# Optimization experiments

Measured on AMD Instinct MI355X. Metric: run time of the kernel, lower is better.

## Reference

```python
import jax, jax.numpy as jnp
import numpy as np

M, N, K, D_IN = 200, 6, 25, 784
GAMMA, EPS = 0.5, 0.5
TOTAL = M * N


def setup_inputs() -> dict:
    key = jax.random.key(0)
    ks = jax.random.split(key, 8)
    B = 16384
    def lin(kk, shape, fan_in):
        bound = 1.0 / np.sqrt(fan_in)
        return jax.random.uniform(kk, shape, jnp.float32, -bound, bound)
    return {
        "batch_x": jax.random.normal(ks[0], (B, D_IN), jnp.float32),
        "Wa": lin(ks[1], (M, D_IN), D_IN),
        "ba": lin(ks[2], (M,), D_IN),
        "Wb": lin(ks[3], (TOTAL, TOTAL), TOTAL),
        "bb": lin(ks[4], (TOTAL,), TOTAL),
        "Wd": lin(ks[5], (D_IN, M), M),
        "bd": lin(ks[6], (D_IN,), M),
    }


def _step(params, carry, x):
    Wa, ba, Wb, bb, Wd, bd = params
    x_b, phi, psi = carry
    # sigma: per-group drive broadcast over cells + full recurrent term, shape (m, n)
    z_a = (Wa @ x + ba)[:, None]                      # (m, 1)
    z_b = (Wb @ x_b + bb).reshape(M, N)               # (m, n)
    sigma = z_a + z_b
    # inhibited activity
    pi = (1.0 - phi) * (sigma - sigma.min() + 1.0)    # (m, n)
    lambda_i = pi.max(axis=1)                         # (m,)
    # top-1 cell per group (scatter of topk indices == one-hot argmax)
    M_pi = jax.nn.one_hot(jnp.argmax(pi, axis=1), N, dtype=sigma.dtype)
    # top-k groups
    _, idx = jax.lax.top_k(lambda_i, K)
    M_lambda = jnp.zeros((M,), sigma.dtype).at[idx].set(1.0)[:, None]
    y = jnp.tanh(M_pi * M_lambda * sigma)             # (m, n)
    x_a_pred = Wd @ y.max(axis=1) + bd                # (D_in,)
    # memory / inhibition updates
    psi_n = jnp.maximum(EPS * psi, y)
    phi_n = jnp.maximum(GAMMA * phi, y)
    alpha = psi_n.sum()
    alpha = jnp.where(alpha == 0.0, 1.0, alpha)
    x_b_n = (psi_n / alpha).reshape(-1)
    # original detaches the recurrent state each step
    carry_n = (jax.lax.stop_gradient(x_b_n),
               jax.lax.stop_gradient(phi_n),
               jax.lax.stop_gradient(psi_n))
    return carry_n, x_a_pred


def reference(batch_x, Wa, ba, Wb, bb, Wd, bd):
    params = (Wa, ba, Wb, bb, Wd, bd)
    carry0 = (jnp.zeros((TOTAL,), batch_x.dtype),
              jnp.zeros((M, N), batch_x.dtype),
              jnp.zeros((M, N), batch_x.dtype))
    (x_b, phi, psi), preds = jax.lax.scan(
        lambda c, x: _step(params, c, x), carry0, batch_x)
    return preds, x_b, phi, psi
```

## Files before the change

### kernel.cpp

```cpp
#include <hip/hip_runtime.h>
#include <math.h>

#define Tn   16384
#define Mg   200
#define Nc   6
#define TOT  1200
#define Kk   25
#define Din  784
#define SP   28

__global__ void transpose_k(const float* __restrict__ src, float* __restrict__ dst,
                            int R, int C) {
    __shared__ float tile[32][33];
    int bx = blockIdx.x * 32, by = blockIdx.y * 32;
    int x = bx + threadIdx.x;
    for (int j = 0; j < 32; j += 8) {
        int y = by + threadIdx.y + j;
        if (x < C && y < R) tile[threadIdx.y + j][threadIdx.x] = src[(size_t)y * C + x];
    }
    __syncthreads();
    int x2 = by + threadIdx.x;
    for (int j = 0; j < 32; j += 8) {
        int y2 = bx + threadIdx.y + j;
        if (x2 < R && y2 < C) dst[(size_t)y2 * R + x2] = tile[threadIdx.x][threadIdx.y + j];
    }
}

__global__ void za_k(const float* __restrict__ X, const float* __restrict__ Wa,
                     const float* __restrict__ ba, float* __restrict__ Za) {
    __shared__ float xs[16][788];
    const int tid = threadIdx.x;
    const int t0  = blockIdx.x * 16;
    for (int idx = tid; idx < 16 * Din; idx += 256) {
        int tt = idx / Din, kk = idx - tt * Din;
        xs[tt][kk] = X[(size_t)(t0 + tt) * Din + kk];
    }
    __syncthreads();
    const int tq = tid & 15, gq = tid >> 4;
    const float4* xrow = reinterpret_cast<const float4*>(&xs[tq][0]);
    for (int g = gq; g < Mg; g += 16) {
        float acc = ba[g];
        const float4* wrow = reinterpret_cast<const float4*>(Wa + (size_t)g * Din);
        for (int k4 = 0; k4 < Din / 4; ++k4) {
            float4 a = xrow[k4], b = wrow[k4];
            acc = fmaf(a.x, b.x, acc); acc = fmaf(a.y, b.y, acc);
            acc = fmaf(a.z, b.z, acc); acc = fmaf(a.w, b.w, acc);
        }
        Za[(size_t)(t0 + tq) * Mg + g] = acc;
    }
}

__launch_bounds__(384, 1)
__global__ void serial_k(const float* __restrict__ Za, const float* __restrict__ WbT,
                         const float* __restrict__ bb,
                         unsigned long long* __restrict__ YP,
                         float* __restrict__ outTail) {
    __shared__ alignas(16) float sigma_sh[50 * SP];
    __shared__ alignas(16) float minp[8];
    __shared__ alignas(16) float selD[32];
    __shared__ alignas(16) int   selO[32];
    __shared__ float alphaS;

    const int tid  = threadIdx.x;
    const int lane = tid & 63;

    if (tid < 64) {
        const bool grp = (lane < 50);
        const int sgb  = lane * SP;
        const int cell0 = 24 * lane;
        const unsigned long long lt = (1ull << lane) - 1ull;

        float ps[24];
        #pragma unroll
        for (int i = 0; i < 24; ++i) ps[i] = 0.f;
        float alpha = 0.f;

        __syncthreads();

        for (int t = 0; t < Tn; ++t) {
            float4 mp4 = *reinterpret_cast<const float4*>(minp);
            float m = fminf(fminf(fminf(mp4.x, mp4.y), fminf(mp4.z, mp4.w)), minp[4]);
            const float m1 = 1.f - m;

            float sg[24];
            if (grp) {
                #pragma unroll
                for (int q = 0; q < 6; ++q) {
                    float4 v = *reinterpret_cast<const float4*>(sigma_sh + sgb + 4 * q);
                    sg[4*q] = v.x; sg[4*q+1] = v.y; sg[4*q+2] = v.z; sg[4*q+3] = v.w;
                }
            } else {
                #pragma unroll
                for (int i = 0; i < 24; ++i) sg[i] = 0.f;
            }

            float bs[4], bp[4]; int bj[4]; unsigned long long kb[4];
            #pragma unroll
            for (int c = 0; c < 4; ++c) { bs[c]=0.f; bp[c]=0.f; bj[c]=0; kb[c]=0ull; }
            if (grp) {
                #pragma unroll
                for (int c = 0; c < 4; ++c) {
                    float best = -INFINITY, sbv = 0.f, pbv = 0.f; int jb = 0;
                    #pragma unroll
                    for (int j = 0; j < 6; ++j) {
                        int i = 6 * c + j;
                        float pv = (1.f - ps[i]) * (sg[i] + m1);
                        bool bet = pv > best;
                        best = bet ? pv : best;
                        jb  = bet ? j : jb;
                        sbv = bet ? sg[i] : sbv;
                        pbv = bet ? ps[i] : pbv;
                    }
                    unsigned ub = __float_as_uint(best);
                    ub ^= (unsigned)(((int)ub) >> 31) | 0x80000000u;
                    int g = 4 * lane + c;
                    kb[c] = ((unsigned long long)ub << 32) |
                            (unsigned long long)(0xFFFFFFFFu - (unsigned)g);
                    bs[c] = sbv; bp[c] = pbv; bj[c] = jb;
                }
            }

            unsigned long long A = 0ull, B = ~0ull;
            unsigned long long p = __shfl(kb[0], 0);
            unsigned long long theta;
            while (true) {
                int cnt = __popcll(__ballot(kb[0] >= p)) + __popcll(__ballot(kb[1] >= p))
                        + __popcll(__ballot(kb[2] >= p)) + __popcll(__ballot(kb[3] >= p));
                if (cnt == Kk) { theta = p; break; }
                if (cnt > Kk) A = p; else B = p;
                unsigned long long m0 = __ballot(kb[0] > A && kb[0] < B);
                unsigned long long m1b = __ballot(kb[1] > A && kb[1] < B);
                unsigned long long m2 = __ballot(kb[2] > A && kb[2] < B);
                unsigned long long m3 = __ballot(kb[3] > A && kb[3] < B);
                int cls; unsigned long long mm;
                if (m0)       { cls = 0; mm = m0; }
                else if (m1b) { cls = 1; mm = m1b; }
                else if (m2)  { cls = 2; mm = m2; }
                else          { cls = 3; mm = m3; }
                int sl = __ffsll(mm) - 1;
                unsigned long long kc = (cls==0)?kb[0]:(cls==1)?kb[1]:(cls==2)?kb[2]:kb[3];
                p = __shfl(kc, sl);
            }

            unsigned long long M0 = __ballot(kb[0] >= theta);
            unsigned long long M1 = __ballot(kb[1] >= theta);
            unsigned long long M2 = __ballot(kb[2] >= theta);
            unsigned long long M3 = __ballot(kb[3] >= theta);
            int base1 = __popcll(M0);
            int base2 = base1 + __popcll(M1);
            int base3 = base2 + __popcll(M2);

            float dsum = 0.f;
            int slotr[4]; unsigned long long yv64[4];
            #pragma unroll
            for (int c = 0; c < 4; ++c) {
                slotr[c] = -1; yv64[c] = 0ull;
                unsigned long long Mc = (c==0)?M0:(c==1)?M1:(c==2)?M2:M3;
                int bse = (c==0)?0:(c==1)?base1:(c==2)?base2:base3;
                bool s = grp && (kb[c] >= theta);
                float d = 0.f;
                if (s) {
                    int slot = bse + __popcll(Mc & lt);
                    float x = fminf(fmaxf(bs[c], -9.f), 9.f);
                    float e = __expf(2.f * x);
                    float y = 1.f - 2.f / (e + 1.f);
                    float yv = fmaxf(y, 0.f);
                    d = fmaxf(y - 0.5f * bp[c], 0.f);
                    int g = 4 * lane + c;
                    selD[slot] = d;
                    selO[slot] = (6 * g + bj[c]) * TOT;
                    slotr[c] = slot;
                    yv64[c] = ((unsigned long long)(unsigned)g << 32) |
                              (unsigned long long)__float_as_uint(yv);
                }
                dsum += d;
                #pragma unroll
                for (int j = 0; j < 6; ++j) {
                    int i = 6 * c + j;
                    float add = (j == bj[c]) ? d : 0.f;
                    ps[i] = fmaf(ps[i], 0.5f, add);
                }
            }
            #pragma unroll
            for (int o = 1; o < 64; o <<= 1) dsum += __shfl_xor(dsum, o);
            alpha = fmaf(alpha, 0.5f, dsum);
            if (lane == 0) alphaS = (alpha == 0.f) ? 1.f : alpha;

            __syncthreads();
            #pragma unroll
            for (int c = 0; c < 4; ++c)
                if (slotr[c] >= 0) YP[(size_t)t * Kk + slotr[c]] = yv64[c];
            __syncthreads();
        }

        if (grp) {
            float inv2 = (alpha == 0.f) ? 1.f : (1.f / alpha);
            #pragma unroll
            for (int i = 0; i < 24; ++i) {
                outTail[cell0 + i]           = ps[i] * inv2;
                outTail[TOT + cell0 + i]     = ps[i];
                outTail[2 * TOT + cell0 + i] = ps[i];
            }
        }
    } else {
        const int j = tid - 64;
        const bool act = (j < 300);
        const int w = (tid >> 6) - 1;
        const int base = act ? 4 * j : 0;
        const int saddr = act ? ((j / 6) * SP + (4 * j) % 24) : 0;
        const int g0 = base / 6, g1 = (base + 3) / 6;
        const bool f1 = ((base + 1) / 6) != g0;
        const bool f2 = ((base + 2) / 6) != g0;
        const bool f3 = ((base + 3) / 6) != g0;

        float4 cb4 = make_float4(0.f, 0.f, 0.f, 0.f);
        if (act) cb4 = *reinterpret_cast<const float4*>(bb + base);
        float za0 = act ? Za[g0] : 0.f;
        float za1 = act ? Za[g1] : 0.f;
        float4 uo = make_float4(0.f, 0.f, 0.f, 0.f);

        {
            float s0 = cb4.x + za0;
            float s1 = cb4.y + (f1 ? za1 : za0);
            float s2 = cb4.z + (f2 ? za1 : za0);
            float s3 = cb4.w + (f3 ? za1 : za0);
            if (act)
                *reinterpret_cast<float4*>(sigma_sh + saddr) = make_float4(s0,s1,s2,s3);
            float lm = act ? fminf(fminf(s0, s1), fminf(s2, s3)) : INFINITY;
            #pragma unroll
            for (int o = 1; o < 64; o <<= 1) lm = fminf(lm, __shfl_xor(lm, o));
            if (lane == 0) minp[w] = lm;
        }
        __syncthreads();

        for (int t = 0; t < Tn; ++t) {
            const int tn = (t + 1 < Tn) ? t + 1 : t;
            float nza0 = act ? Za[(size_t)tn * Mg + g0] : 0.f;
            float nza1 = act ? Za[(size_t)tn * Mg + g1] : 0.f;
            uo.x *= 0.5f; uo.y *= 0.5f; uo.z *= 0.5f; uo.w *= 0.5f;

            __syncthreads();

            float vD = 0.f; int vO = 0;
            if (lane < 25) { vD = selD[lane]; vO = selO[lane]; }
            const float av  = alphaS;
            const float inv = 1.f / av;

            float4 cc[Kk];
            #pragma unroll
            for (int k = 0; k < Kk; ++k) {
                int offk = __builtin_amdgcn_readlane(vO, k);
                cc[k] = *reinterpret_cast<const float4*>(WbT + offk + base);
            }
            __builtin_amdgcn_sched_barrier(0);
            #pragma unroll
            for (int k = 0; k < Kk; ++k) {
                float dk = __uint_as_float(
                    (unsigned)__builtin_amdgcn_readlane((int)__float_as_uint(vD), k));
                uo.x = fmaf(dk, cc[k].x, uo.x);
                uo.y = fmaf(dk, cc[k].y, uo.y);
                uo.z = fmaf(dk, cc[k].z, uo.z);
                uo.w = fmaf(dk, cc[k].w, uo.w);
            }

            float s0 = fmaf(uo.x, inv, cb4.x + nza0);
            float s1 = fmaf(uo.y, inv, cb4.y + (f1 ? nza1 : nza0));
            float s2 = fmaf(uo.z, inv, cb4.z + (f2 ? nza1 : nza0));
            float s3 = fmaf(uo.w, inv, cb4.w + (f3 ? nza1 : nza0));
            if (act)
                *reinterpret_cast<float4*>(sigma_sh + saddr) = make_float4(s0,s1,s2,s3);
            float lm = act ? fminf(fminf(s0, s1), fminf(s2, s3)) : INFINITY;
            #pragma unroll
            for (int o = 1; o < 64; o <<= 1) lm = fminf(lm, __shfl_xor(lm, o));
            if (lane == 0) minp[w] = lm;

            __syncthreads();
        }
    }
}

__global__ void preds_k(const unsigned long long* __restrict__ YP,
                        const float* __restrict__ WdT, const float* __restrict__ bd,
                        float* __restrict__ out) {
    const int t = blockIdx.x;
    __shared__ float sv[Kk];
    __shared__ int   si[Kk];
    if (threadIdx.x < Kk) {
        unsigned long long v = YP[(size_t)t * Kk + threadIdx.x];
        sv[threadIdx.x] = __uint_as_float((unsigned)v);
        si[threadIdx.x] = (int)(v >> 32);
    }
    __syncthreads();
    for (int d = threadIdx.x; d < Din; d += 256) {
        float acc = bd[d];
        #pragma unroll
        for (int k = 0; k < Kk; ++k)
            acc = fmaf(sv[k], WdT[(size_t)si[k] * Din + d], acc);
        out[(size_t)t * Din + d] = acc;
    }
}

extern "C" void kernel_launch(void* const* d_in, const int* in_sizes, int n_in,
                              void* d_out, int out_size, void* d_ws, size_t ws_size,
                              hipStream_t stream) {
    const float* X  = (const float*)d_in[0];
    const float* Wa = (const float*)d_in[1];
    const float* ba = (const float*)d_in[2];
    const float* Wb = (const float*)d_in[3];
    const float* bb = (const float*)d_in[4];
    const float* Wd = (const float*)d_in[5];
    const float* bd = (const float*)d_in[6];
    float* out = (float*)d_out;

    float* w    = (float*)d_ws;
    float* Za   = w;
    float* WbT  = Za  + (size_t)Tn * Mg;
    float* WdT  = WbT + (size_t)TOT * TOT;
    unsigned long long* YP =
        (unsigned long long*)(WdT + (size_t)Mg * Din);

    dim3 tb(32, 8);
    transpose_k<<<dim3((TOT + 31) / 32, (TOT + 31) / 32), tb, 0, stream>>>(Wb, WbT, TOT, TOT);
    transpose_k<<<dim3((Mg + 31) / 32, (Din + 31) / 32), tb, 0, stream>>>(Wd, WdT, Din, Mg);
    za_k<<<Tn / 16, 256, 0, stream>>>(X, Wa, ba, Za);
    serial_k<<<1, 384, 0, stream>>>(Za, WbT, bb, YP, out + (size_t)Tn * Din);
    preds_k<<<Tn, 256, 0, stream>>>(YP, WdT, bd, out);
}
```

Before: 72.82 ms.

## Shorten serial top-k wave critical path by moving alpha reduction and deferring stores

The selection wavefront no longer computes the alpha reduction. Each consumer wave now recomputes alpha from the selected d values, overlapping that work with the WbT gather loads. The YP global stores are deferred into the next iteration, and the psi decay update is moved after the barrier. The top-k threshold search is warm-started from the previous step's threshold instead of lane 0's key. Together these shorten the serial per-step critical path of the recurrent scan, at the cost of duplicated reductions and a more complex barrier protocol.

```diff
diff --git a/kernel.cpp b/kernel.cpp
--- a/kernel.cpp
+++ b/kernel.cpp
@@ -73,11 +73,21 @@
         float ps[24];
         #pragma unroll
         for (int i = 0; i < 24; ++i) ps[i] = 0.f;
-        float alpha = 0.f;
+        unsigned long long thw = 0ull;
+        int slotr[4] = {-1, -1, -1, -1};
+        unsigned long long yv64[4] = {0ull, 0ull, 0ull, 0ull};
+        int bj[4] = {0, 0, 0, 0};
+        float dcl[4] = {0.f, 0.f, 0.f, 0.f};
 
         __syncthreads();
 
         for (int t = 0; t < Tn; ++t) {
+            if (t > 0) {
+                #pragma unroll
+                for (int c = 0; c < 4; ++c)
+                    if (slotr[c] >= 0) YP[(size_t)(t - 1) * Kk + slotr[c]] = yv64[c];
+            }
+
             float4 mp4 = *reinterpret_cast<const float4*>(minp);
             float m = fminf(fminf(fminf(mp4.x, mp4.y), fminf(mp4.z, mp4.w)), minp[4]);
             const float m1 = 1.f - m;
@@ -94,7 +104,7 @@
                 for (int i = 0; i < 24; ++i) sg[i] = 0.f;
             }
 
-            float bs[4], bp[4]; int bj[4]; unsigned long long kb[4];
+            float bs[4], bp[4]; unsigned long long kb[4];
             #pragma unroll
             for (int c = 0; c < 4; ++c) { bs[c]=0.f; bp[c]=0.f; bj[c]=0; kb[c]=0ull; }
             if (grp) {
@@ -121,7 +131,7 @@
             }
 
             unsigned long long A = 0ull, B = ~0ull;
-            unsigned long long p = __shfl(kb[0], 0);
+            unsigned long long p = thw;
             unsigned long long theta;
             while (true) {
                 int cnt = __popcll(__ballot(kb[0] >= p)) + __popcll(__ballot(kb[1] >= p))
@@ -141,6 +151,7 @@
                 unsigned long long kc = (cls==0)?kb[0]:(cls==1)?kb[1]:(cls==2)?kb[2]:kb[3];
                 p = __shfl(kc, sl);
             }
+            thw = theta;
 
             unsigned long long M0 = __ballot(kb[0] >= theta);
             unsigned long long M1 = __ballot(kb[1] >= theta);
@@ -150,11 +161,9 @@
             int base2 = base1 + __popcll(M1);
             int base3 = base2 + __popcll(M2);
 
-            float dsum = 0.f;
-            int slotr[4]; unsigned long long yv64[4];
             #pragma unroll
             for (int c = 0; c < 4; ++c) {
-                slotr[c] = -1; yv64[c] = 0ull;
+                slotr[c] = -1;
                 unsigned long long Mc = (c==0)?M0:(c==1)?M1:(c==2)?M2:M3;
                 int bse = (c==0)?0:(c==1)?base1:(c==2)?base2:base3;
                 bool s = grp && (kb[c] >= theta);
@@ -173,28 +182,32 @@
                     yv64[c] = ((unsigned long long)(unsigned)g << 32) |
                               (unsigned long long)__float_as_uint(yv);
                 }
-                dsum += d;
-                #pragma unroll
-                for (int j = 0; j < 6; ++j) {
-                    int i = 6 * c + j;
-                    float add = (j == bj[c]) ? d : 0.f;
-                    ps[i] = fmaf(ps[i], 0.5f, add);
+                dcl[c] = d;
+            }
+
+            __syncthreads();
+
+            if (grp) {
+                #pragma unroll
+                for (int c = 0; c < 4; ++c) {
+                    #pragma unroll
+                    for (int j = 0; j < 6; ++j) {
+                        int i = 6 * c + j;
+                        float add = (j == bj[c]) ? dcl[c] : 0.f;
+                        ps[i] = fmaf(ps[i], 0.5f, add);
+                    }
                 }
             }
-            #pragma unroll
-            for (int o = 1; o < 64; o <<= 1) dsum += __shfl_xor(dsum, o);
-            alpha = fmaf(alpha, 0.5f, dsum);
-            if (lane == 0) alphaS = (alpha == 0.f) ? 1.f : alpha;
 
             __syncthreads();
-            #pragma unroll
-            for (int c = 0; c < 4; ++c)
-                if (slotr[c] >= 0) YP[(size_t)t * Kk + slotr[c]] = yv64[c];
-            __syncthreads();
-        }
-
+        }
+
+        #pragma unroll
+        for (int c = 0; c < 4; ++c)
+            if (slotr[c] >= 0) YP[(size_t)(Tn - 1) * Kk + slotr[c]] = yv64[c];
         if (grp) {
-            float inv2 = (alpha == 0.f) ? 1.f : (1.f / alpha);
+            float a = alphaS;
+            float inv2 = (a == 0.f) ? 1.f : (1.f / a);
             #pragma unroll
             for (int i = 0; i < 24; ++i) {
                 outTail[cell0 + i]           = ps[i] * inv2;
@@ -215,11 +228,12 @@
 
         float4 cb4 = make_float4(0.f, 0.f, 0.f, 0.f);
         if (act) cb4 = *reinterpret_cast<const float4*>(bb + base);
-        float za0 = act ? Za[g0] : 0.f;
-        float za1 = act ? Za[g1] : 0.f;
         float4 uo = make_float4(0.f, 0.f, 0.f, 0.f);
+        float alpha = 0.f;
 
         {
+            float za0 = act ? Za[g0] : 0.f;
+            float za1 = act ? Za[g1] : 0.f;
             float s0 = cb4.x + za0;
             float s1 = cb4.y + (f1 ? za1 : za0);
             float s2 = cb4.z + (f2 ? za1 : za0);
@@ -234,18 +248,16 @@
         __syncthreads();
 
         for (int t = 0; t < Tn; ++t) {
+            uo.x *= 0.5f; uo.y *= 0.5f; uo.z *= 0.5f; uo.w *= 0.5f;
+
+            __syncthreads();
+
+            float vD = 0.f; int vO = 0;
+            if (lane < 25) { vD = selD[lane]; vO = selO[lane]; }
+
             const int tn = (t + 1 < Tn) ? t + 1 : t;
             float nza0 = act ? Za[(size_t)tn * Mg + g0] : 0.f;
             float nza1 = act ? Za[(size_t)tn * Mg + g1] : 0.f;
-            uo.x *= 0.5f; uo.y *= 0.5f; uo.z *= 0.5f; uo.w *= 0.5f;
-
-            __syncthreads();
-
-            float vD = 0.f; int vO = 0;
-            if (lane < 25) { vD = selD[lane]; vO = selO[lane]; }
-            const float av  = alphaS;
-            const float inv = 1.f / av;
-
             float4 cc[Kk];
             #pragma unroll
             for (int k = 0; k < Kk; ++k) {
@@ -253,6 +265,15 @@
                 cc[k] = *reinterpret_cast<const float4*>(WbT + offk + base);
             }
             __builtin_amdgcn_sched_barrier(0);
+
+            float av = vD;
+            #pragma unroll
+            for (int o = 1; o < 64; o <<= 1) av += __shfl_xor(av, o);
+            alpha = fmaf(alpha, 0.5f, av);
+            const float A0  = (alpha == 0.f) ? 1.f : alpha;
+            const float inv = 1.f / A0;
+            if (w == 0 && lane == 0) alphaS = alpha;
+
             #pragma unroll
             for (int k = 0; k < Kk; ++k) {
                 float dk = __uint_as_float(
```

After: 71.35 ms, median of 2. -2.0%, faster.
